# Performance work log

Measured on AMD Instinct MI355X. Metric: run time of the kernel, lower is better.

The kernel has to match this reference:

```python
import jax, jax.numpy as jnp
import numpy as np
from jax import lax

Q = 3          # Self-ONN polynomial order
EPS = 1e-5     # InstanceNorm1d eps


def setup_inputs() -> dict:
    key = jax.random.key(0)
    k1, k2, k3 = jax.random.split(key, 3)
    B, Cin, L = 16, 128, 8192
    Cout, K = 128, 3
    x = jax.random.normal(k1, (B, Cin, L), dtype=jnp.float32)
    # Conv1d weight over power-expanded channels: [Cout, Cin*Q, K]
    W = jax.random.normal(k2, (Cout, Cin * Q, K), dtype=jnp.float32) * 0.05
    b = jax.random.normal(k3, (Cout,), dtype=jnp.float32) * 0.05
    return {"x": x, "W": W, "b": b}


def reference(x, W, b):
    x = jnp.repeat(x, 2, axis=-1)
    # Self-ONN power expansion: concat x^1..x^Q along channel dim -> (B, C*Q, 2L)
    powers = jnp.concatenate([x ** (i + 1) for i in range(Q)], axis=1)
    # Conv1d, stride 1, padding 1 (same length)
    out = lax.conv_general_dilated(
        powers, W,
        window_strides=(1,),
        padding=[(1, 1)],
        dimension_numbers=("NCH", "OIH", "NCH"),
    ) + b[None, :, None]
    # InstanceNorm1d (affine=False): normalize over length per (batch, channel)
    mean = jnp.mean(out, axis=-1, keepdims=True)
    var = jnp.var(out, axis=-1, keepdims=True)
    out = (out - mean) * lax.rsqrt(var + EPS)
    # Tanh activation (self.relu is nn.Tanh()); dropout=False -> no-op
    return jnp.tanh(out)
```

## Files before the change

kernel.cpp:

```cpp
#include <hip/hip_runtime.h>
#include <hip/hip_fp16.h>
#include <math.h>

#define BATCH 16
#define CIN   128
#define LIN   8192
#define COUT  128
#define LOUT  16384
#define KEXP  768
#define NT    256
#define NTILES (LIN/NT)
#define PCOLS 258
#define PCPAD 136
#define PSZ   (PCOLS*PCPAD)

typedef _Float16 f16x8 __attribute__((ext_vector_type(8)));
typedef float    f32x4 __attribute__((ext_vector_type(4)));

__global__ void prep_weights(const float* __restrict__ W,
                             _Float16* __restrict__ WE,
                             _Float16* __restrict__ WO) {
  int idx = blockIdx.x * 256 + threadIdx.x;
  int co = idx / KEXP;
  int k  = idx % KEXP;
  int sh = (k >= 384) ? 1 : 0;
  int cq = k - 384 * sh;
  const float* w = W + ((size_t)co * 384 + cq) * 3;
  float we, wo;
  if (sh == 0) { we = w[0];        wo = w[0] + w[1]; }
  else         { we = w[1] + w[2]; wo = w[2];        }
  int q  = cq >> 7;
  int c  = cq & 127;
  int ks = q * 8 + sh * 4 + (c >> 5);
  int kk = c & 31, quad = kk >> 3, j = kk & 7;
  int mtile = co >> 4, l15 = co & 15;
  size_t off = ((size_t)((mtile * 24 + ks) * 64) + quad * 16 + l15) * 8 + j;
  WE[off] = (_Float16)we;
  WO[off] = (_Float16)wo;
}


#define AFLOAD(DST, KS) do {                                               \
  _Pragma("unroll")                                                        \
  for (int fm = 0; fm < 4; ++fm) {                                         \
    int mt = wm * 4 + fm;                                                  \
    DST[fm] = *(const f16x8*)(Wsel + ((size_t)((mt * 24 + (KS)) * 64) + lane) * 8); \
  }                                                                        \
} while (0)

#define BFLOAD(DST, CUR, S) do {                                           \
  const _Float16* pb = (CUR) + (((S) & 3) * 32) + kl;                      \
  const int shft = (((S) >> 2) + isO);                                     \
  _Pragma("unroll")                                                        \
  for (int fn = 0; fn < 8; ++fn) {                                         \
    int colB = wn * 128 + fn * 16 + l15 + shft;                            \
    DST[fn] = *(const f16x8*)(pb + colB * PCPAD);                          \
  }                                                                        \
} while (0)

#define BUILD_P2() do {                                                    \
  _Pragma("unroll")                                                        \
  for (int slot = 0; slot < 9; ++slot) {                                   \
    if (slot < 8 || t < PCOLS * 16 - 4096) {                               \
      int task = t + 512 * slot;                                           \
      int g    = task / PCOLS;                                             \
      int col  = task - g * PCOLS;                                         \
      int off  = col * PCPAD + g * 8;                                      \
      f16x8 v = *(f16x8*)(planes + off);                                   \
      *(f16x8*)(planes + PSZ + off) = v * v;                               \
    }                                                                      \
  }                                                                        \
} while (0)

#define BUILD_P3() do {                                                    \
  _Pragma("unroll")                                                        \
  for (int slot = 0; slot < 9; ++slot) {                                   \
    if (slot < 8 || t < PCOLS * 16 - 4096) {                               \
      int task = t + 512 * slot;                                           \
      int g    = task / PCOLS;                                             \
      int col  = task - g * PCOLS;                                         \
      int off  = col * PCPAD + g * 8;                                      \
      f16x8 v1 = *(f16x8*)(planes + off);                                  \
      f16x8 v2 = *(f16x8*)(planes + PSZ + off);                            \
      *(f16x8*)(planes + off) = v1 * v2;                                   \
    }                                                                      \
  }                                                                        \
} while (0)

__launch_bounds__(512, 2)
__global__ void conv_gemm(const float* __restrict__ x,
                          const _Float16* __restrict__ WE,
                          const _Float16* __restrict__ WO,
                          float* __restrict__ out,
                          float* __restrict__ stats) {
  extern __shared__ char smem[];
  float*    sstats = (float*)smem;
  _Float16* planes = (_Float16*)(smem + 1024);

  const int tile = blockIdx.x;
  const int b    = blockIdx.y;
  const int i0   = tile * NT;
  const int t    = threadIdx.x;
  const int lane = t & 63;
  const int wave = t >> 6;
  const int isO  = wave & 1;
  const int wn   = (wave >> 1) & 1;
  const int wm   = wave >> 2;
  const int l15  = lane & 15, quad = lane >> 4;
  const int kl   = quad * 8;

  if (t < 128) { sstats[2 * t] = 0.f; sstats[2 * t + 1] = 0.f; }

  const float* xb = x + (size_t)b * CIN * LIN;
  const _Float16* Wsel = isO ? WO : WE;

  f32x4 acc[4][8];
  const f32x4 zero = {0.f, 0.f, 0.f, 0.f};
#pragma unroll
  for (int fm = 0; fm < 4; ++fm)
#pragma unroll
    for (int fn = 0; fn < 8; ++fn) acc[fm][fn] = zero;

  f16x8 af[2][4], bf[2][8];
  AFLOAD(af[0], 0);

#pragma unroll
  for (int slot = 0; slot < 9; ++slot) {
    const bool tval = (slot < 8) || (t < PCOLS * 16 - 4096);
    int task = t + 512 * slot;
    int g    = task / PCOLS;
    int col  = task - g * PCOLS;
    int gi   = i0 - 1 + col;
    const bool ok = tval && gi >= 0 && gi < LIN;
    const float* px = xb + (size_t)g * 8 * LIN + gi;
    f16x8 w1;
#pragma unroll
    for (int j = 0; j < 8; ++j) {
      float v = ok ? px[(size_t)j * LIN] : 0.f;
      w1[j] = (_Float16)v;
    }
    if (tval) *(f16x8*)(planes + col * PCPAD + g * 8) = w1;
  }
  __syncthreads();

#pragma unroll
  for (int q = 0; q < 3; ++q) {
    _Float16* cur = planes + ((q == 1) ? PSZ : 0);
    BFLOAD(bf[0], cur, 0);
#pragma unroll
    for (int s = 0; s < 8; ++s) {
      const int ks = q * 8 + s;
      if (ks + 1 < 24) AFLOAD(af[(ks + 1) & 1], ks + 1);
      if (s + 1 < 8)   BFLOAD(bf[(s + 1) & 1], cur, s + 1);
      __builtin_amdgcn_s_setprio(1);
#pragma unroll
      for (int fm = 0; fm < 4; ++fm)
#pragma unroll
        for (int fn = 0; fn < 8; ++fn)
          acc[fm][fn] = __builtin_amdgcn_mfma_f32_16x16x32_f16(af[ks & 1][fm], bf[s & 1][fn], acc[fm][fn], 0, 0, 0);
      __builtin_amdgcn_s_setprio(0);
      if (s == 0 && q == 0) BUILD_P2();
      if (s == 0 && q == 1) BUILD_P3();
    }
    __syncthreads();
  }

  float* orow_base = out + (size_t)b * COUT * LOUT + isO;
#pragma unroll
  for (int fm = 0; fm < 4; ++fm) {
#pragma unroll
    for (int r = 0; r < 4; ++r) {
      float s1 = 0.f, s2 = 0.f;
#pragma unroll
      for (int fn = 0; fn < 8; ++fn) {
        float v = acc[fm][fn][r];
        s1 += v;
        s2 += v * v;
      }
#pragma unroll
      for (int off = 8; off >= 1; off >>= 1) {
        s1 += __shfl_xor(s1, off, 64);
        s2 += __shfl_xor(s2, off, 64);
      }
      int co = wm * 64 + fm * 16 + quad * 4 + r;
      if (l15 == 0) {
        atomicAdd(&sstats[2 * co], s1);
        atomicAdd(&sstats[2 * co + 1], s2);
      }
      float* orow = orow_base + (size_t)co * LOUT;
#pragma unroll
      for (int fn = 0; fn < 8; ++fn) {
        int n = i0 + wn * 128 + fn * 16 + l15;
        orow[2 * n] = acc[fm][fn][r];
      }
    }
  }
  __syncthreads();
  if (t < 128) {
    atomicAdd(&stats[((size_t)b * COUT + t) * 2],     sstats[2 * t]);
    atomicAdd(&stats[((size_t)b * COUT + t) * 2 + 1], sstats[2 * t + 1]);
  }
}

__device__ inline float tanh_fast(float z) {
  float e = __expf(2.f * z);
  return 1.f - 2.f * __builtin_amdgcn_rcpf(e + 1.f);
}

__global__ void norm_tanh(float* __restrict__ out, const float* __restrict__ stats) {
  int row  = blockIdx.x >> 1;
  int half = blockIdx.x & 1;
  float s1 = stats[2 * row], s2 = stats[2 * row + 1];
  const float invN = 1.f / (float)LOUT;
  float mean = s1 * invN;
  float var  = fmaxf(s2 * invN - mean * mean, 0.f);
  float inv  = rsqrtf(var + 1e-5f);
  float c0   = -mean * inv;
  float4* p = (float4*)(out + (size_t)row * LOUT) + half * (LOUT / 8);
  for (int i = threadIdx.x; i < LOUT / 8; i += 256) {
    float4 v = p[i];
    v.x = tanh_fast(fmaf(v.x, inv, c0));
    v.y = tanh_fast(fmaf(v.y, inv, c0));
    v.z = tanh_fast(fmaf(v.z, inv, c0));
    v.w = tanh_fast(fmaf(v.w, inv, c0));
    p[i] = v;
  }
}

extern "C" void kernel_launch(void* const* d_in, const int* in_sizes, int n_in,
                              void* d_out, int out_size, void* d_ws, size_t ws_size,
                              hipStream_t stream) {
  const float* x = (const float*)d_in[0];
  const float* W = (const float*)d_in[1];
  float* out = (float*)d_out;

  float*    stats = (float*)d_ws;
  _Float16* WE    = (_Float16*)((char*)d_ws + 16384);
  _Float16* WO    = WE + (size_t)COUT * KEXP;

  hipMemsetAsync(d_ws, 0, 16384, stream);
  prep_weights<<<dim3((COUT * KEXP) / 256), dim3(256), 0, stream>>>(W, WE, WO);

  size_t shmem = 1024 + (size_t)PSZ * 2 * 2;
  hipFuncSetAttribute(reinterpret_cast<const void*>(conv_gemm),
                      hipFuncAttributeMaxDynamicSharedMemorySize, (int)shmem);
  conv_gemm<<<dim3(NTILES, BATCH), dim3(512), shmem, stream>>>(x, WE, WO, out, stats);

  norm_tanh<<<dim3(2 * BATCH * COUT), dim3(256), 0, stream>>>(out, stats);
}
```

Measured before the change: 328.7 us.

## Stage GEMM output through LDS for coalesced stores, split B fragments to cut registers

The conv GEMM epilogue now writes accumulators into shared memory, reusing the planes region, in two halves interleaved by even/odd parity. It then issues fully coalesced 16-byte global stores, replacing the old strided scalar stores with stride 2. The B-fragment double buffer is split into two half-loads of 4 fragments, interleaved with two MFMA groups, to lower register pressure. The norm_tanh loop is unrolled to batch 4 float4 loads per thread. Together these aim to reduce uncoalesced write traffic and VGPR usage, at the cost of extra barriers and an LDS round trip.

```diff
diff --git a/kernel.cpp b/kernel.cpp
--- a/kernel.cpp
+++ b/kernel.cpp
@@ -48,13 +48,13 @@
   }                                                                        \
 } while (0)
 
-#define BFLOAD(DST, CUR, S) do {                                           \
+#define BFLOAD4(DST, CUR, S, H) do {                                       \
   const _Float16* pb = (CUR) + (((S) & 3) * 32) + kl;                      \
   const int shft = (((S) >> 2) + isO);                                     \
   _Pragma("unroll")                                                        \
-  for (int fn = 0; fn < 8; ++fn) {                                         \
-    int colB = wn * 128 + fn * 16 + l15 + shft;                            \
-    DST[fn] = *(const f16x8*)(pb + colB * PCPAD);                          \
+  for (int f4 = 0; f4 < 4; ++f4) {                                         \
+    int colB = wn * 128 + ((H) * 4 + f4) * 16 + l15 + shft;                \
+    DST[f4] = *(const f16x8*)(pb + colB * PCPAD);                          \
   }                                                                        \
 } while (0)
 
@@ -96,6 +96,7 @@
   extern __shared__ char smem[];
   float*    sstats = (float*)smem;
   _Float16* planes = (_Float16*)(smem + 1024);
+  float*    abuf   = (float*)(smem + 1024);
 
   const int tile = blockIdx.x;
   const int b    = blockIdx.y;
@@ -121,7 +122,7 @@
 #pragma unroll
     for (int fn = 0; fn < 8; ++fn) acc[fm][fn] = zero;
 
-  f16x8 af[2][4], bf[2][8];
+  f16x8 af[2][4], bf[2][4];
   AFLOAD(af[0], 0);
 
 #pragma unroll
@@ -142,30 +143,38 @@
     if (tval) *(f16x8*)(planes + col * PCPAD + g * 8) = w1;
   }
   __syncthreads();
+  BFLOAD4(bf[0], planes, 0, 0);
 
 #pragma unroll
   for (int q = 0; q < 3; ++q) {
     _Float16* cur = planes + ((q == 1) ? PSZ : 0);
-    BFLOAD(bf[0], cur, 0);
 #pragma unroll
     for (int s = 0; s < 8; ++s) {
       const int ks = q * 8 + s;
       if (ks + 1 < 24) AFLOAD(af[(ks + 1) & 1], ks + 1);
-      if (s + 1 < 8)   BFLOAD(bf[(s + 1) & 1], cur, s + 1);
+      BFLOAD4(bf[1], cur, s, 1);
       __builtin_amdgcn_s_setprio(1);
 #pragma unroll
       for (int fm = 0; fm < 4; ++fm)
 #pragma unroll
-        for (int fn = 0; fn < 8; ++fn)
-          acc[fm][fn] = __builtin_amdgcn_mfma_f32_16x16x32_f16(af[ks & 1][fm], bf[s & 1][fn], acc[fm][fn], 0, 0, 0);
+        for (int f4 = 0; f4 < 4; ++f4)
+          acc[fm][f4] = __builtin_amdgcn_mfma_f32_16x16x32_f16(af[ks & 1][fm], bf[0][f4], acc[fm][f4], 0, 0, 0);
       __builtin_amdgcn_s_setprio(0);
       if (s == 0 && q == 0) BUILD_P2();
       if (s == 0 && q == 1) BUILD_P3();
+      if (s < 7) BFLOAD4(bf[0], cur, s + 1, 0);
+      __builtin_amdgcn_s_setprio(1);
+#pragma unroll
+      for (int fm = 0; fm < 4; ++fm)
+#pragma unroll
+        for (int f4 = 0; f4 < 4; ++f4)
+          acc[fm][4 + f4] = __builtin_amdgcn_mfma_f32_16x16x32_f16(af[ks & 1][fm], bf[1][f4], acc[fm][4 + f4], 0, 0, 0);
+      __builtin_amdgcn_s_setprio(0);
     }
     __syncthreads();
-  }
-
-  float* orow_base = out + (size_t)b * COUT * LOUT + isO;
+    if (q < 2) BFLOAD4(bf[0], planes + ((q == 0) ? PSZ : 0), 0, 0);
+  }
+
 #pragma unroll
   for (int fm = 0; fm < 4; ++fm) {
 #pragma unroll
@@ -182,20 +191,39 @@
         s1 += __shfl_xor(s1, off, 64);
         s2 += __shfl_xor(s2, off, 64);
       }
-      int co = wm * 64 + fm * 16 + quad * 4 + r;
       if (l15 == 0) {
+        int co = wm * 64 + fm * 16 + quad * 4 + r;
         atomicAdd(&sstats[2 * co], s1);
         atomicAdd(&sstats[2 * co + 1], s2);
       }
-      float* orow = orow_base + (size_t)co * LOUT;
-#pragma unroll
-      for (int fn = 0; fn < 8; ++fn) {
-        int n = i0 + wn * 128 + fn * 16 + l15;
-        orow[2 * n] = acc[fm][fn][r];
-      }
-    }
-  }
-  __syncthreads();
+    }
+  }
+
+#pragma unroll
+  for (int pm = 0; pm < 2; ++pm) {
+    __syncthreads();
+    if (wm == pm) {
+#pragma unroll
+      for (int fm = 0; fm < 4; ++fm)
+#pragma unroll
+        for (int r = 0; r < 4; ++r) {
+          int lr = fm * 16 + quad * 4 + r;
+#pragma unroll
+          for (int fn = 0; fn < 8; ++fn) {
+            int lc = wn * 128 + fn * 16 + l15;
+            abuf[lr * 512 + 2 * lc + isO] = acc[fm][fn][r];
+          }
+        }
+    }
+    __syncthreads();
+    float* dstbase = out + (size_t)b * COUT * LOUT + (size_t)(pm * 64) * LOUT + 2 * i0;
+#pragma unroll
+    for (int it = 0; it < 16; ++it) {
+      int c  = t + it * 512;
+      int cr = c >> 7, pos = c & 127;
+      *(f32x4*)(dstbase + (size_t)cr * LOUT + pos * 4) = *(const f32x4*)(abuf + cr * 512 + pos * 4);
+    }
+  }
   if (t < 128) {
     atomicAdd(&stats[((size_t)b * COUT + t) * 2],     sstats[2 * t]);
     atomicAdd(&stats[((size_t)b * COUT + t) * 2 + 1], sstats[2 * t + 1]);
@@ -217,13 +245,20 @@
   float inv  = rsqrtf(var + 1e-5f);
   float c0   = -mean * inv;
   float4* p = (float4*)(out + (size_t)row * LOUT) + half * (LOUT / 8);
-  for (int i = threadIdx.x; i < LOUT / 8; i += 256) {
-    float4 v = p[i];
-    v.x = tanh_fast(fmaf(v.x, inv, c0));
-    v.y = tanh_fast(fmaf(v.y, inv, c0));
-    v.z = tanh_fast(fmaf(v.z, inv, c0));
-    v.w = tanh_fast(fmaf(v.w, inv, c0));
-    p[i] = v;
+#pragma unroll
+  for (int mi = 0; mi < 2; ++mi) {
+    float4 v[4];
+#pragma unroll
+    for (int u = 0; u < 4; ++u) v[u] = p[threadIdx.x + 256 * (mi * 4 + u)];
+#pragma unroll
+    for (int u = 0; u < 4; ++u) {
+      v[u].x = tanh_fast(fmaf(v[u].x, inv, c0));
+      v[u].y = tanh_fast(fmaf(v[u].y, inv, c0));
+      v[u].z = tanh_fast(fmaf(v[u].z, inv, c0));
+      v[u].w = tanh_fast(fmaf(v[u].w, inv, c0));
+    }
+#pragma unroll
+    for (int u = 0; u < 4; ++u) p[threadIdx.x + 256 * (mi * 4 + u)] = v[u];
   }
 }
 
```

After: 327.4 us. About the same (-0.4%).
